# Optimization experiments

Measured on AMD Instinct MI355X. Metric: run time of the kernel, lower is better.

Reference implementation:

```python
import jax, jax.numpy as jnp
import numpy as np

N_NODES = 100000
N_EDGES = 1600000
IN_DIM = 64
HIDDEN = 128
N_CLASSES = 16


def setup_inputs() -> dict:
    key = jax.random.key(0)
    ks = jax.random.split(key, 16)
    inp = {
        'feats': jax.random.normal(ks[0], (N_NODES, IN_DIM), dtype=jnp.float32),
        'H1_src': jax.random.randint(ks[1], (N_EDGES,), 0, N_NODES),
        'H1_dst': jax.random.randint(ks[2], (N_EDGES,), 0, N_NODES),
        'H2_src': jax.random.randint(ks[3], (N_EDGES,), 0, N_NODES),
        'H2_dst': jax.random.randint(ks[4], (N_EDGES,), 0, N_NODES),
        'W1_self1': 0.1 * jax.random.normal(ks[5], (IN_DIM, HIDDEN), dtype=jnp.float32),
        'W1_neigh1': 0.1 * jax.random.normal(ks[6], (IN_DIM, HIDDEN), dtype=jnp.float32),
        'W1_self2': 0.1 * jax.random.normal(ks[7], (HIDDEN, HIDDEN), dtype=jnp.float32),
        'W1_neigh2': 0.1 * jax.random.normal(ks[8], (HIDDEN, HIDDEN), dtype=jnp.float32),
        'W1_lin': 0.1 * jax.random.normal(ks[9], (HIDDEN, N_CLASSES), dtype=jnp.float32),
        'W2_self1': 0.1 * jax.random.normal(ks[10], (IN_DIM, HIDDEN), dtype=jnp.float32),
        'W2_neigh1': 0.1 * jax.random.normal(ks[11], (IN_DIM, HIDDEN), dtype=jnp.float32),
        'W2_self2': 0.1 * jax.random.normal(ks[12], (HIDDEN, HIDDEN), dtype=jnp.float32),
        'W2_neigh2': 0.1 * jax.random.normal(ks[13], (HIDDEN, HIDDEN), dtype=jnp.float32),
        'W2_lin': 0.1 * jax.random.normal(ks[14], (HIDDEN, N_CLASSES), dtype=jnp.float32),
    }
    return inp


def _neighbor_mean(x, src, dst, n_nodes):
    # gather messages along edges, sum into destinations, divide by in-degree
    msg = x[src]                                        # [E, d] irregular gather
    agg = jax.ops.segment_sum(msg, dst, num_segments=n_nodes)  # [N, d]
    deg = jax.ops.segment_sum(jnp.ones((src.shape[0],), x.dtype), dst,
                              num_segments=n_nodes)     # [N]
    return agg / jnp.maximum(deg, 1.0)[:, None]         # zero-degree nodes -> 0


def _sage_layer(x, src, dst, W_self, W_neigh):
    h_neigh = _neighbor_mean(x, src, dst, x.shape[0])
    return jax.nn.relu(x @ W_self + h_neigh @ W_neigh)


def _graphsage(src, dst, x, Ws1, Wn1, Ws2, Wn2, Wlin):
    h = _sage_layer(x, src, dst, Ws1, Wn1)
    h = _sage_layer(h, src, dst, Ws2, Wn2)
    graph_rep = jnp.mean(h, axis=0)                     # dgl.mean_nodes (single graph)
    return jax.nn.sigmoid(graph_rep @ Wlin)             # [num_classes]


def reference(feats, H1_src, H1_dst, H2_src, H2_dst,
              W1_self1, W1_neigh1, W1_self2, W1_neigh2, W1_lin,
              W2_self1, W2_neigh1, W2_self2, W2_neigh2, W2_lin):
    rep1 = _graphsage(H1_src, H1_dst, feats, W1_self1, W1_neigh1, W1_self2, W1_neigh2, W1_lin)
    rep2 = _graphsage(H2_src, H2_dst, feats, W2_self1, W2_neigh1, W2_self2, W2_neigh2, W2_lin)
    return (rep1 + rep2) / 2.0
```

## Files before the change

kernel.cpp:

```cpp
#include <hip/hip_runtime.h>
#include <hip/hip_fp16.h>

#define NN 100000
#define NE 1600000
#define IND 64
#define HID 128
#define NCLS 16
#define GEMMB (NN / 16)
#define RBLK 50
#define NCRS 98
#define CAPC 18432
#define CAPF 352
#define NDCAP 48
#define EPB1 16384
#define NBG1 ((NE + EPB1 - 1) / EPB1)

typedef float v2f __attribute__((ext_vector_type(2)));
typedef __attribute__((ext_vector_type(8))) short short8v;
typedef __attribute__((ext_vector_type(4))) float f32x4;

__device__ __forceinline__ float fp8_sw_unpack(unsigned b) {
    unsigned s = (b >> 7) & 1u, em = b & 0x7fu;
    return __uint_as_float((s << 31) | (em << 20)) * 0x1p+120f;
}
__device__ __forceinline__ unsigned fp8_sw_pack(float f) {
    float c = fminf(fmaxf(f, -448.f), 448.f) * 0x1p-120f;
    unsigned b = __float_as_uint(c);
    unsigned s = b >> 31; b &= 0x7fffffffu;
    b = b + 0x7ffffu + ((b >> 20) & 1u);
    unsigned em = b >> 20;
    if (em > 0x7eu) em = 0x7eu;
    return (s << 7) | em;
}
template<bool HI>
__device__ __forceinline__ unsigned pk8(float a, float b, unsigned old) {
#if __has_builtin(__builtin_amdgcn_cvt_pk_fp8_f32)
    return (unsigned)__builtin_amdgcn_cvt_pk_fp8_f32(a, b, (int)old, HI);
#else
    unsigned v = fp8_sw_pack(a) | (fp8_sw_pack(b) << 8);
    return HI ? ((old & 0x0000ffffu) | (v << 16)) : ((old & 0xffff0000u) | v);
#endif
}
template<bool HI>
__device__ __forceinline__ v2f upk8(unsigned u) {
#if __has_builtin(__builtin_amdgcn_cvt_pk_f32_fp8)
    return __builtin_amdgcn_cvt_pk_f32_fp8((int)u, HI);
#else
    unsigned x = HI ? (u >> 16) : u;
    v2f r; r.x = fp8_sw_unpack(x & 0xffu); r.y = fp8_sw_unpack((x >> 8) & 0xffu);
    return r;
#endif
}

__device__ __forceinline__ short f2bf(float f) {
    unsigned u = __float_as_uint(f);
    return (short)((u + 0x7fffu + ((u >> 16) & 1u)) >> 16);
}

__device__ __forceinline__ void bacc8v(v2f* a, uint4 v) {
    a[0] += upk8<false>(v.x); a[1] += upk8<true>(v.x);
    a[2] += upk8<false>(v.y); a[3] += upk8<true>(v.y);
    a[4] += upk8<false>(v.z); a[5] += upk8<true>(v.z);
    a[6] += upk8<false>(v.w); a[7] += upk8<true>(v.w);
}

__device__ __forceinline__ short8v mk8(const v2f* a, float iv) {
    short8v r;
    r[0] = f2bf(a[0].x * iv); r[1] = f2bf(a[0].y * iv);
    r[2] = f2bf(a[1].x * iv); r[3] = f2bf(a[1].y * iv);
    r[4] = f2bf(a[2].x * iv); r[5] = f2bf(a[2].y * iv);
    r[6] = f2bf(a[3].x * iv); r[7] = f2bf(a[3].y * iv);
    return r;
}

__global__ void conv16_kernel(const float4* __restrict__ x, uint4* __restrict__ o, int n16) {
    int i = blockIdx.x * blockDim.x + threadIdx.x;
    if (i >= n16) return;
    float4 v0 = x[4 * i + 0], v1 = x[4 * i + 1], v2 = x[4 * i + 2], v3 = x[4 * i + 3];
    uint4 u;
    u.x = pk8<true>(v0.z, v0.w, pk8<false>(v0.x, v0.y, 0u));
    u.y = pk8<true>(v1.z, v1.w, pk8<false>(v1.x, v1.y, 0u));
    u.z = pk8<true>(v2.z, v2.w, pk8<false>(v2.x, v2.y, 0u));
    u.w = pk8<true>(v3.z, v3.w, pk8<false>(v3.x, v3.y, 0u));
    o[i] = u;
}

__global__ void packW_all(const float* __restrict__ Ws1a, const float* __restrict__ Wn1a,
                          const float* __restrict__ Ws1b, const float* __restrict__ Wn1b,
                          const float* __restrict__ Ws2a, const float* __restrict__ Wn2a,
                          const float* __restrict__ Ws2b, const float* __restrict__ Wn2b,
                          short* __restrict__ out) {
    int t = blockIdx.x * 256 + threadIdx.x;
    if (t >= 12288) return;
    const float *Ws, *Wn; short* o; int KS;
    if (t < 2048)      { Ws = Ws1a; Wn = Wn1a; o = out;         KS = 64;  }
    else if (t < 4096) { Ws = Ws1b; Wn = Wn1b; o = out + 16384; KS = 64;  t -= 2048; }
    else if (t < 8192) { Ws = Ws2a; Wn = Wn2a; o = out + 32768; KS = 128; t -= 4096; }
    else               { Ws = Ws2b; Wn = Wn2b; o = out + 65536; KS = 128; t -= 8192; }
    int l = t & 63, f = t >> 6, nn = f & 7, kk = f >> 3;
    int col = nn * 16 + (l & 15);
    int k0 = kk * 32 + ((l >> 4) * 8);
    unsigned short v[8];
#pragma unroll
    for (int j = 0; j < 8; j++) {
        int k = k0 + j;
        float x = (k < KS) ? Ws[k * 128 + col] : Wn[(k - KS) * 128 + col];
        v[j] = (unsigned short)f2bf(x);
    }
    uint4 u;
    u.x = (unsigned)v[0] | ((unsigned)v[1] << 16);
    u.y = (unsigned)v[2] | ((unsigned)v[3] << 16);
    u.z = (unsigned)v[4] | ((unsigned)v[5] << 16);
    u.w = (unsigned)v[6] | ((unsigned)v[7] << 16);
    ((uint4*)o)[t] = u;
}

__global__ __launch_bounds__(512) void place_coarse(
    const int* __restrict__ s0, const int* __restrict__ d0,
    const int* __restrict__ s1, const int* __restrict__ d1,
    int* __restrict__ gcurC,
    unsigned* __restrict__ pc0, unsigned* __restrict__ pc1) {
    __shared__ int h[NCRS], hb[NCRS];
    const int bi = blockIdx.x;
    const int g = bi >= NBG1;
    const int* src = g ? s1 : s0;
    const int* dst = g ? d1 : d0;
    unsigned* pc = g ? pc1 : pc0;
    const int base = (g ? bi - NBG1 : bi) * EPB1;
    for (int i = threadIdx.x; i < NCRS; i += 512) h[i] = 0;
    __syncthreads();
    for (int j = 0; j < EPB1; j += 512) {
        int e = base + j + threadIdx.x;
        if (e < NE) atomicAdd(&h[dst[e] >> 10], 1);
    }
    __syncthreads();
    for (int i = threadIdx.x; i < NCRS; i += 512) {
        hb[i] = h[i] ? atomicAdd(&gcurC[g * NCRS + i], h[i]) : 0;
        h[i] = 0;
    }
    __syncthreads();
    for (int j = 0; j < EPB1; j += 512) {
        int e = base + j + threadIdx.x;
        if (e < NE) {
            int d = dst[e];
            int b = d >> 10;
            int slot = atomicAdd(&h[b], 1);
            int idx = hb[b] + slot;
            if (idx < CAPC)
                pc[(size_t)b * CAPC + idx] = (unsigned)src[e] | ((unsigned)(d & 1023) << 17);
        }
    }
}

__global__ __launch_bounds__(512) void place_fine(
    const unsigned* __restrict__ pc0, const unsigned* __restrict__ pc1,
    const int* __restrict__ gcurC,
    unsigned* __restrict__ pf0, unsigned* __restrict__ pf1,
    int* __restrict__ fcnt0, int* __restrict__ fcnt1) {
    __shared__ int h2[64], cur2[64];
    const int bi = blockIdx.x;
    const int g = bi >= NCRS;
    const int c = g ? bi - NCRS : bi;
    const unsigned* pc = g ? pc1 : pc0;
    unsigned* pf = g ? pf1 : pf0;
    int* fcnt = g ? fcnt1 : fcnt0;
    int ecnt = gcurC[g * NCRS + c];
    if (ecnt > CAPC) ecnt = CAPC;
    const size_t cb = (size_t)c * CAPC;
    const int tid = threadIdx.x;
    if (tid < 64) h2[tid] = 0;
    __syncthreads();
    for (int e = tid; e < ecnt; e += 512)
        atomicAdd(&h2[(pc[cb + e] >> 21) & 63], 1);
    __syncthreads();
    if (tid < 64) {
        int v = h2[tid];
        fcnt[c * 64 + tid] = v > CAPF ? CAPF : v;
        cur2[tid] = 0;
    }
    __syncthreads();
    for (int e = tid; e < ecnt; e += 512) {
        unsigned u = pc[cb + e];
        int sub = (u >> 21) & 63;
        int pos = atomicAdd(&cur2[sub], 1);
        if (pos < CAPF)
            pf[(size_t)(c * 64 + sub) * CAPF + pos] = (u & 0x1FFFFu) | (((u >> 17) & 15u) << 17);
    }
}

template<int KS, bool REDUCE>
__global__ __launch_bounds__(256) void sage_fused(
    const float* __restrict__ xin,
    const unsigned* __restrict__ x8a, const unsigned* __restrict__ x8b,
    const unsigned* __restrict__ pf0, const unsigned* __restrict__ pf1,
    const int* __restrict__ fcnt0, const int* __restrict__ fcnt1,
    const short* __restrict__ Wfa, const short* __restrict__ Wfb,
    float* __restrict__ outRa, float* __restrict__ outRb,
    unsigned* __restrict__ outHa, unsigned* __restrict__ outHb) {
    constexpr int KT = (2 * KS) / 32;
    __shared__ short8v sA[KT * 64];
    __shared__ float otile[REDUCE ? 1 : 16 * 132];
    __shared__ int lcnt[16];
    __shared__ int ssrcL[16 * NDCAP];

    const int tid = threadIdx.x;
    const int g = blockIdx.x >= GEMMB;
    const int gid = g ? blockIdx.x - GEMMB : blockIdx.x;
    const int n0 = gid * 16;
    const unsigned* x8 = g ? x8b : x8a;
    const unsigned* pf = g ? pf1 : pf0;
    const int* fcnt = g ? fcnt1 : fcnt0;
    const short8v* Wf = (const short8v*)(g ? Wfb : Wfa);
    const uint4* xb4 = (const uint4*)x8;

    if (tid < 16) lcnt[tid] = 0;
    __syncthreads();

    {
        int ecnt = fcnt[gid];
        for (int e = tid; e < ecnt; e += 256) {
            unsigned u = pf[(size_t)gid * CAPF + e];
            int loc = (u >> 17) & 15;
            int pos = atomicAdd(&lcnt[loc], 1);
            if (pos < NDCAP) ssrcL[loc * NDCAP + pos] = (int)(u & 0x1FFFFu);
        }
    }

    if (tid < 128) {
        if constexpr (KS == IND) {
            int node = tid >> 3, r = tid & 7;
            float4 v0 = ((const float4*)xin)[(size_t)(n0 + node) * 16 + r * 2];
            float4 v1 = ((const float4*)xin)[(size_t)(n0 + node) * 16 + r * 2 + 1];
            short8v s;
            s[0] = f2bf(v0.x); s[1] = f2bf(v0.y); s[2] = f2bf(v0.z); s[3] = f2bf(v0.w);
            s[4] = f2bf(v1.x); s[5] = f2bf(v1.y); s[6] = f2bf(v1.z); s[7] = f2bf(v1.w);
            int kk = r >> 2, kg = r & 3;
            sA[(kk * 64 + kg * 16 + node) ^ (kk & 7)] = s;
        } else {
            int node = tid >> 3, c8 = tid & 7;
            uint4 u = xb4[(size_t)(n0 + node) * 8 + c8];
            v2f a[8];
            a[0] = upk8<false>(u.x); a[1] = upk8<true>(u.x);
            a[2] = upk8<false>(u.y); a[3] = upk8<true>(u.y);
            a[4] = upk8<false>(u.z); a[5] = upk8<true>(u.z);
            a[6] = upk8<false>(u.w); a[7] = upk8<true>(u.w);
            int kk = c8 >> 1, kg0 = (c8 & 1) * 2;
            sA[(kk * 64 + kg0 * 16 + node) ^ (kk & 7)]       = mk8(a, 1.0f);
            sA[(kk * 64 + (kg0 + 1) * 16 + node) ^ (kk & 7)] = mk8(a + 4, 1.0f);
        }
    }
    __syncthreads();

    {
        const int nb = tid >> 4;
        const int degt = lcnt[nb];
        const int degc = degt > NDCAP ? NDCAP : degt;
        const int* L = &ssrcL[nb * NDCAP];
        v2f a[8];
#pragma unroll
        for (int j = 0; j < 8; j++) a[j] = (v2f)(0.0f);

        if constexpr (KS == HID) {
            const int l = tid & 7;
            const int h = (tid >> 3) & 1;
            int i = h;
            for (; i + 2 < degc; i += 4) {
                int i0 = L[i], i1 = L[i + 2];
                uint4 v0 = xb4[(size_t)i0 * 8 + l];
                uint4 v1 = xb4[(size_t)i1 * 8 + l];
                bacc8v(a, v0);
                bacc8v(a, v1);
            }
            if (i < degc) bacc8v(a, xb4[(size_t)L[i] * 8 + l]);
#pragma unroll
            for (int j = 0; j < 8; j++) {
                a[j].x += __shfl_xor(a[j].x, 8);
                a[j].y += __shfl_xor(a[j].y, 8);
            }
            if (h == 0) {
                float iv = 1.0f / fmaxf((float)degt, 1.0f);
                int kk = 4 + (l >> 1), kg0 = (l & 1) * 2;
                sA[(kk * 64 + kg0 * 16 + nb) ^ (kk & 7)]       = mk8(a, iv);
                sA[(kk * 64 + (kg0 + 1) * 16 + nb) ^ (kk & 7)] = mk8(a + 4, iv);
            }
        } else {
            const int sub = tid & 15;
            const int l = sub & 3;
            const int h = sub >> 2;
            int i = h;
            for (; i + 4 < degc; i += 8) {
                int i0 = L[i], i1 = L[i + 4];
                uint4 v0 = xb4[(size_t)i0 * 4 + l];
                uint4 v1 = xb4[(size_t)i1 * 4 + l];
                bacc8v(a, v0);
                bacc8v(a, v1);
            }
            if (i < degc) bacc8v(a, xb4[(size_t)L[i] * 4 + l]);
#pragma unroll
            for (int j = 0; j < 8; j++) {
                a[j].x += __shfl_xor(a[j].x, 4);
                a[j].y += __shfl_xor(a[j].y, 4);
            }
#pragma unroll
            for (int j = 0; j < 8; j++) {
                a[j].x += __shfl_xor(a[j].x, 8);
                a[j].y += __shfl_xor(a[j].y, 8);
            }
            if (h == 0) {
                float iv = 1.0f / fmaxf((float)degt, 1.0f);
                int kk = 2 + (l >> 1), kg0 = (l & 1) * 2;
                sA[(kk * 64 + kg0 * 16 + nb) ^ (kk & 7)]       = mk8(a, iv);
                sA[(kk * 64 + (kg0 + 1) * 16 + nb) ^ (kk & 7)] = mk8(a + 4, iv);
            }
        }
    }
    __syncthreads();

    const int lane = tid & 63;
    const int q = tid >> 6;
    const int r15 = lane & 15;
    const int kg = lane >> 4;
    f32x4 acc0 = {0.f, 0.f, 0.f, 0.f};
    f32x4 acc1 = {0.f, 0.f, 0.f, 0.f};

#pragma unroll
    for (int kk = 0; kk < KT; kk++) {
        short8v af = sA[(kk * 64 + lane) ^ (kk & 7)];
        short8v b0 = Wf[(kk * 8 + 2 * q + 0) * 64 + lane];
        short8v b1 = Wf[(kk * 8 + 2 * q + 1) * 64 + lane];
        acc0 = __builtin_amdgcn_mfma_f32_16x16x32_bf16(af, b0, acc0, 0, 0, 0);
        acc1 = __builtin_amdgcn_mfma_f32_16x16x32_bf16(af, b1, acc1, 0, 0, 0);
    }

    if constexpr (!REDUCE) {
#pragma unroll
        for (int i = 0; i < 4; i++) {
            otile[(kg * 4 + i) * 132 + 32 * q + r15]      = fmaxf(acc0[i], 0.f);
            otile[(kg * 4 + i) * 132 + 32 * q + 16 + r15] = fmaxf(acc1[i], 0.f);
        }
        __syncthreads();
        int node = tid >> 4, c = tid & 15;
        float4 x0 = *(const float4*)&otile[node * 132 + c * 8];
        float4 x1 = *(const float4*)&otile[node * 132 + c * 8 + 4];
        unsigned w0 = pk8<false>(x0.x, x0.y, 0u); w0 = pk8<true>(x0.z, x0.w, w0);
        unsigned w1 = pk8<false>(x1.x, x1.y, 0u); w1 = pk8<true>(x1.z, x1.w, w1);
        uint2* o8 = (uint2*)(g ? outHb : outHa);
        o8[(size_t)(n0 + node) * 16 + c] = make_uint2(w0, w1);
    } else {
        float s0 = 0.f, s1 = 0.f;
#pragma unroll
        for (int i = 0; i < 4; i++) {
            s0 += fmaxf(acc0[i], 0.f);
            s1 += fmaxf(acc1[i], 0.f);
        }
        s0 += __shfl_xor(s0, 16); s0 += __shfl_xor(s0, 32);
        s1 += __shfl_xor(s1, 16); s1 += __shfl_xor(s1, 32);
        float* outR = g ? outRb : outRa;
        size_t base = (size_t)gid * 128;
        if (lane < 16)      outR[base + 32 * q + lane] = s0;
        else if (lane < 32) outR[base + 32 * q + 16 + (lane & 15)] = s1;
    }
}

__global__ void reduce1_kernel(const float* __restrict__ p0, const float* __restrict__ p1,
                               float* __restrict__ p2) {
    const int bb = blockIdx.x;
    const int tid = threadIdx.x;
    const int g = tid >> 7;
    const int col = tid & 127;
    const float* p = g ? p1 : p0;
    const int per = GEMMB / RBLK;
    float s = 0.0f;
    for (int r = 0; r < per; r++) s += p[(size_t)(bb * per + r) * 128 + col];
    p2[(size_t)bb * 256 + tid] = s;
}

__global__ void final_kernel(const float* __restrict__ p2,
                             const float* __restrict__ Wlin1,
                             const float* __restrict__ Wlin2,
                             float* __restrict__ out) {
    __shared__ float rep[2][HID];
    __shared__ float sg[32];
    const int tid = threadIdx.x;
    float s = 0.0f;
    for (int r = 0; r < RBLK; r++) s += p2[r * 256 + tid];
    rep[tid >> 7][tid & 127] = s * (1.0f / (float)NN);
    __syncthreads();
    if (tid < 32) {
        const int g = tid / 16;
        const int c = tid % 16;
        const float* W = g ? Wlin2 : Wlin1;
        float a = 0.0f;
        for (int k = 0; k < HID; k++) a += rep[g][k] * W[k * NCLS + c];
        sg[tid] = 1.0f / (1.0f + expf(-a));
    }
    __syncthreads();
    if (tid < 16) out[tid] = 0.5f * (sg[tid] + sg[16 + tid]);
}

extern "C" void kernel_launch(void* const* d_in, const int* in_sizes, int n_in,
                              void* d_out, int out_size, void* d_ws, size_t ws_size,
                              hipStream_t stream) {
    const float* feats = (const float*)d_in[0];
    const int* srcp[2] = {(const int*)d_in[1], (const int*)d_in[3]};
    const int* dstp[2] = {(const int*)d_in[2], (const int*)d_in[4]};
    const float* Ws1[2] = {(const float*)d_in[5], (const float*)d_in[10]};
    const float* Wn1[2] = {(const float*)d_in[6], (const float*)d_in[11]};
    const float* Ws2[2] = {(const float*)d_in[7], (const float*)d_in[12]};
    const float* Wn2[2] = {(const float*)d_in[8], (const float*)d_in[13]};
    const float* Wlin[2] = {(const float*)d_in[9], (const float*)d_in[14]};

    char* w = (char*)d_ws;
    unsigned* fb8 = (unsigned*)w;   w += (size_t)NN * IND;
    unsigned* h18a = (unsigned*)w;  w += (size_t)NN * HID;
    unsigned* h18b = (unsigned*)w;  w += (size_t)NN * HID;
    unsigned* pf0 = (unsigned*)w;   w += (size_t)GEMMB * CAPF * 4;
    unsigned* pf1 = (unsigned*)w;   w += (size_t)GEMMB * CAPF * 4;
    float* part0 = (float*)w;       w += (size_t)GEMMB * 128 * 4;
    float* part1 = (float*)w;       w += (size_t)GEMMB * 128 * 4;
    float* p2 = (float*)w;          w += (size_t)RBLK * 256 * 4;
    int* fcnt0 = (int*)w;           w += (size_t)NCRS * 64 * 4;
    int* fcnt1 = (int*)w;           w += (size_t)NCRS * 64 * 4;
    int* gcurC = (int*)w;           w += 2 * NCRS * 4;
    w = (char*)(((uintptr_t)w + 15) & ~(uintptr_t)15);
    short* wpk = (short*)w;         w += 98304 * 2;
    unsigned* pc0 = h18a;
    unsigned* pc1 = h18b;

    conv16_kernel<<<(NN * IND / 16 + 255) / 256, 256, 0, stream>>>(
        (const float4*)feats, (uint4*)fb8, NN * IND / 16);

    packW_all<<<48, 256, 0, stream>>>(Ws1[0], Wn1[0], Ws1[1], Wn1[1],
                                      Ws2[0], Wn2[0], Ws2[1], Wn2[1], wpk);

    (void)hipMemsetAsync(gcurC, 0, 2 * NCRS * 4, stream);
    place_coarse<<<2 * NBG1, 512, 0, stream>>>(srcp[0], dstp[0], srcp[1], dstp[1],
                                               gcurC, pc0, pc1);
    place_fine<<<2 * NCRS, 512, 0, stream>>>(pc0, pc1, gcurC, pf0, pf1, fcnt0, fcnt1);

    sage_fused<IND, false><<<2 * GEMMB, 256, 0, stream>>>(
        feats, fb8, fb8, pf0, pf1, fcnt0, fcnt1,
        wpk, wpk + 16384,
        nullptr, nullptr, h18a, h18b);

    sage_fused<HID, true><<<2 * GEMMB, 256, 0, stream>>>(
        nullptr, h18a, h18b, pf0, pf1, fcnt0, fcnt1,
        wpk + 32768, wpk + 65536,
        part0, part1, nullptr, nullptr);

    reduce1_kernel<<<RBLK, 256, 0, stream>>>(part0, part1, p2);
    final_kernel<<<1, 256, 0, stream>>>(p2, Wlin[0], Wlin[1], (float*)d_out);
}
```

Baseline: 317.6 us.

## Stage bucketed edges in LDS to coalesce global scatter writes

Both partitioning kernels (coarse and fine bucketing of edges by destination) now first sort each chunk of edges into shared memory using a local histogram and prefix scan. Each wave then writes contiguous runs per bucket to global memory, replacing scattered per-edge stores. The coarse pass halves edges per block to fit the LDS buffer, and the fine pass processes chunks of 8192. This adds extra syncs and LDS traffic, and raises LDS use per block, which may lower occupancy.

```diff
diff --git a/kernel.cpp b/kernel.cpp
--- a/kernel.cpp
+++ b/kernel.cpp
@@ -12,8 +12,9 @@
 #define CAPC 18432
 #define CAPF 352
 #define NDCAP 48
-#define EPB1 16384
+#define EPB1 8192
 #define NBG1 ((NE + EPB1 - 1) / EPB1)
+#define FCH 8192
 
 typedef float v2f __attribute__((ext_vector_type(2)));
 typedef __attribute__((ext_vector_type(8))) short short8v;
@@ -120,35 +121,49 @@
     const int* __restrict__ s1, const int* __restrict__ d1,
     int* __restrict__ gcurC,
     unsigned* __restrict__ pc0, unsigned* __restrict__ pc1) {
-    __shared__ int h[NCRS], hb[NCRS];
+    __shared__ unsigned ebuf[EPB1];
+    __shared__ int h[128], off[128];
+    __shared__ int hb[NCRS];
     const int bi = blockIdx.x;
     const int g = bi >= NBG1;
     const int* src = g ? s1 : s0;
     const int* dst = g ? d1 : d0;
     unsigned* pc = g ? pc1 : pc0;
     const int base = (g ? bi - NBG1 : bi) * EPB1;
-    for (int i = threadIdx.x; i < NCRS; i += 512) h[i] = 0;
-    __syncthreads();
-    for (int j = 0; j < EPB1; j += 512) {
-        int e = base + j + threadIdx.x;
-        if (e < NE) atomicAdd(&h[dst[e] >> 10], 1);
-    }
-    __syncthreads();
-    for (int i = threadIdx.x; i < NCRS; i += 512) {
-        hb[i] = h[i] ? atomicAdd(&gcurC[g * NCRS + i], h[i]) : 0;
-        h[i] = 0;
-    }
-    __syncthreads();
-    for (int j = 0; j < EPB1; j += 512) {
-        int e = base + j + threadIdx.x;
-        if (e < NE) {
-            int d = dst[e];
-            int b = d >> 10;
-            int slot = atomicAdd(&h[b], 1);
-            int idx = hb[b] + slot;
-            if (idx < CAPC)
-                pc[(size_t)b * CAPC + idx] = (unsigned)src[e] | ((unsigned)(d & 1023) << 17);
-        }
+    const int tid = threadIdx.x;
+    int nle = NE - base; if (nle > EPB1) nle = EPB1;
+
+    if (tid < 128) h[tid] = 0;
+    __syncthreads();
+    for (int j = tid; j < nle; j += 512) atomicAdd(&h[dst[base + j] >> 10], 1);
+    __syncthreads();
+    if (tid < 128) off[tid] = h[tid];
+    __syncthreads();
+    for (int o = 1; o < 128; o <<= 1) {
+        int v = (tid < 128 && tid >= o) ? off[tid - o] : 0;
+        __syncthreads();
+        if (tid < 128) off[tid] += v;
+        __syncthreads();
+    }
+    if (tid < NCRS) hb[tid] = h[tid] ? atomicAdd(&gcurC[g * NCRS + tid], h[tid]) : 0;
+    __syncthreads();
+    if (tid < 128) h[tid] = off[tid] - h[tid];
+    __syncthreads();
+    for (int j = tid; j < nle; j += 512) {
+        int d = dst[base + j];
+        int b = d >> 10;
+        int pos = atomicAdd(&h[b], 1);
+        ebuf[pos] = (unsigned)src[base + j] | ((unsigned)(d & 1023) << 17);
+    }
+    __syncthreads();
+    const int wv = tid >> 6, lane = tid & 63;
+    for (int b = wv; b < NCRS; b += 8) {
+        int beg = b ? off[b - 1] : 0;
+        int run = off[b] - beg;
+        int gb = hb[b];
+        if (gb + run > CAPC) run = CAPC - gb;
+        for (int i = lane; i < run; i += 64)
+            pc[(size_t)b * CAPC + gb + i] = ebuf[beg + i];
     }
 }
 
@@ -157,7 +172,8 @@
     const int* __restrict__ gcurC,
     unsigned* __restrict__ pf0, unsigned* __restrict__ pf1,
     int* __restrict__ fcnt0, int* __restrict__ fcnt1) {
-    __shared__ int h2[64], cur2[64];
+    __shared__ unsigned obuf[FCH];
+    __shared__ int h2[64], off2[64], cur2[64], gcur2[64];
     const int bi = blockIdx.x;
     const int g = bi >= NCRS;
     const int c = g ? bi - NCRS : bi;
@@ -168,23 +184,49 @@
     if (ecnt > CAPC) ecnt = CAPC;
     const size_t cb = (size_t)c * CAPC;
     const int tid = threadIdx.x;
-    if (tid < 64) h2[tid] = 0;
-    __syncthreads();
-    for (int e = tid; e < ecnt; e += 512)
-        atomicAdd(&h2[(pc[cb + e] >> 21) & 63], 1);
-    __syncthreads();
+    const int wv = tid >> 6, lane = tid & 63;
+
+    if (tid < 64) gcur2[tid] = 0;
+    __syncthreads();
+    for (int s = 0; s < ecnt; s += FCH) {
+        int n = ecnt - s; if (n > FCH) n = FCH;
+        if (tid < 64) h2[tid] = 0;
+        __syncthreads();
+        for (int e = tid; e < n; e += 512)
+            atomicAdd(&h2[(pc[cb + s + e] >> 21) & 63], 1);
+        __syncthreads();
+        if (tid < 64) off2[tid] = h2[tid];
+        __syncthreads();
+        for (int o = 1; o < 64; o <<= 1) {
+            int v = (tid < 64 && tid >= o) ? off2[tid - o] : 0;
+            __syncthreads();
+            if (tid < 64) off2[tid] += v;
+            __syncthreads();
+        }
+        if (tid < 64) cur2[tid] = off2[tid] - h2[tid];
+        __syncthreads();
+        for (int e = tid; e < n; e += 512) {
+            unsigned u = pc[cb + s + e];
+            int sub = (u >> 21) & 63;
+            int pos = atomicAdd(&cur2[sub], 1);
+            obuf[pos] = (u & 0x1FFFFu) | (((u >> 17) & 15u) << 17);
+        }
+        __syncthreads();
+        for (int sub = wv; sub < 64; sub += 8) {
+            int beg = sub ? off2[sub - 1] : 0;
+            int run = off2[sub] - beg;
+            int gb = gcur2[sub];
+            if (gb + run > CAPF) run = CAPF - gb;
+            for (int i = lane; i < run; i += 64)
+                pf[(size_t)(c * 64 + sub) * CAPF + gb + i] = obuf[beg + i];
+        }
+        __syncthreads();
+        if (tid < 64) gcur2[tid] += h2[tid];
+        __syncthreads();
+    }
     if (tid < 64) {
-        int v = h2[tid];
+        int v = gcur2[tid];
         fcnt[c * 64 + tid] = v > CAPF ? CAPF : v;
-        cur2[tid] = 0;
-    }
-    __syncthreads();
-    for (int e = tid; e < ecnt; e += 512) {
-        unsigned u = pc[cb + e];
-        int sub = (u >> 21) & 63;
-        int pos = atomicAdd(&cur2[sub], 1);
-        if (pos < CAPF)
-            pf[(size_t)(c * 64 + sub) * CAPF + pos] = (u & 0x1FFFFu) | (((u >> 17) & 15u) << 17);
     }
 }
 
```

New measurement: 306.0 us. 3.7% less time.
